# Kernel tuning notes

Hardware: AMD Instinct MI355X
Metric: run time of the kernel (lower is better)

## Reference

```python
import jax, jax.numpy as jnp
import numpy as np

DEST = 64          # args['output_size']
NET = 256          # network_size = input_size - 3*dest_size
INPUT = NET + 3 * DEST  # 448
B, N = 4, 2048


def setup_inputs() -> dict:
    key = jax.random.key(0)
    ks = jax.random.split(key, 9)
    node_feature = jax.random.normal(ks[0], (B, N, INPUT), jnp.float32)
    adj_forward = jax.random.uniform(ks[1], (B, N, N), jnp.float32)
    adj_backward = jax.random.uniform(ks[2], (B, N, N), jnp.float32)
    s = 1.0 / np.sqrt(2 * DEST)
    Wf = jax.random.normal(ks[3], (2 * DEST, DEST), jnp.float32) * s
    bf = jnp.zeros((DEST,), jnp.float32)
    Wb = jax.random.normal(ks[4], (2 * DEST, DEST), jnp.float32) * s
    bb = jnp.zeros((DEST,), jnp.float32)
    W_emb = jax.random.normal(ks[5], (NET, 2 * DEST), jnp.float32) / np.sqrt(NET)
    b_emb = jnp.zeros((2 * DEST,), jnp.float32)
    return {"node_feature": node_feature, "adj_forward": adj_forward,
            "adj_backward": adj_backward, "Wf": Wf, "bf": bf,
            "Wb": Wb, "bb": bb, "W_emb": W_emb, "b_emb": b_emb}


def _gcn(x, adj, W, b):
    # GCN layer: aggregate neighbors then project. x: [B,N,2d], adj: [B,N,N]
    h = jnp.einsum('bmn,bnf->bmf', adj, x)  # message passing
    return h @ W + b                         # [B,N,d]


def reference(node_feature, adj_forward, adj_backward, Wf, bf, Wb, bb, W_emb, b_emb):
    dyn = node_feature[:, :, :DEST]                 # [B,N,d]
    struct = node_feature[:, :, DEST:3 * DEST]      # [B,N,2d]
    stat = node_feature[:, :, 3 * DEST:]            # [B,N,NET]
    fwd_code = dyn * _gcn(struct, adj_forward, Wf, bf)
    bwd_code = dyn * _gcn(struct, adj_backward, Wb, bb)
    emb = jnp.concatenate((fwd_code, bwd_code), axis=2)  # [B,N,2d]
    gate = jax.nn.sigmoid(stat @ W_emb + b_emb)           # [B,N,2d]
    return emb * gate
```

## Files before the change

### kernel.cpp

```cpp
#include <hip/hip_runtime.h>
#include <hip/hip_bf16.h>
#include <math.h>

#define BB   4
#define NN   2048
#define INPT 448

typedef float f32x4 __attribute__((ext_vector_type(4)));
typedef short s16x8 __attribute__((ext_vector_type(8)));
typedef unsigned int u32;

#define MFMA(a,b,c) __builtin_amdgcn_mfma_f32_16x16x32_bf16((a),(b),(c),0,0,0)

__device__ __align__(16) unsigned short g_WcatF[4*8*64*8];
__device__ __align__(16) unsigned short g_WembF[8*8*64*8];
__device__ __align__(16) unsigned short g_UtF[BB*2*64*4*64*8];
__device__ __align__(16) float          g_G2[BB*NN*128];

__device__ __forceinline__ u32 bf16pk(float a, float b) {
    u32 ua = __builtin_bit_cast(u32, a);
    u32 ub = __builtin_bit_cast(u32, b);
    ua += 0x7fffu + ((ua >> 16) & 1u);
    ub += 0x7fffu + ((ub >> 16) & 1u);
    return (ua >> 16) | (ub & 0xffff0000u);
}
__device__ __forceinline__ unsigned short bf16b(float a) {
    u32 ua = __builtin_bit_cast(u32, a);
    ua += 0x7fffu + ((ua >> 16) & 1u);
    return (unsigned short)(ua >> 16);
}

__global__ void k_weights(const float* __restrict__ Wf, const float* __restrict__ Wb,
                          const float* __restrict__ We) {
    int t = blockIdx.x * 256 + threadIdx.x;
    if (t < 2048) {
        int l = t & 63, jf = (t >> 6) & 7, kg = t >> 9;
        int j  = jf * 16 + (l & 15);
        int f0 = kg * 32 + (l >> 4) * 8;
        union { u32 u[4]; s16x8 s; } r;
        #pragma unroll
        for (int e = 0; e < 8; e += 2) {
            float v0 = (j < 64) ? Wf[(f0 + e    ) * 64 + j] : Wb[(f0 + e    ) * 64 + (j - 64)];
            float v1 = (j < 64) ? Wf[(f0 + e + 1) * 64 + j] : Wb[(f0 + e + 1) * 64 + (j - 64)];
            r.u[e >> 1] = bf16pk(v0, v1);
        }
        *(s16x8*)&g_WcatF[t * 8] = r.s;
    } else if (t < 2048 + 4096) {
        int idx = t - 2048;
        int l = idx & 63, cf = (idx >> 6) & 7, kg = idx >> 9;
        int c  = cf * 16 + (l & 15);
        int k0 = kg * 32 + (l >> 4) * 8;
        union { u32 u[4]; s16x8 s; } r;
        #pragma unroll
        for (int e = 0; e < 8; e += 2)
            r.u[e >> 1] = bf16pk(We[(k0 + e) * 128 + c], We[(k0 + e + 1) * 128 + c]);
        *(s16x8*)&g_WembF[idx * 8] = r.s;
    }
}

__global__ __launch_bounds__(256) void k_prep(const float* __restrict__ nfeat,
                                              const float* __restrict__ bemb) {
    __shared__ __align__(16) char sm[24576];
    int tid = threadIdx.x;
    int w = tid >> 6, l = tid & 63, lr = l & 15, lc = l >> 4;
    int bid = blockIdx.x;

    if (bid < 256) {
        int b = bid >> 6, nb = bid & 63;
        unsigned short* ss = (unsigned short*)sm;
        unsigned short* ob = (unsigned short*)(sm + 8192);
        const float* base = nfeat + (size_t)(b * NN + nb * 32) * INPT;
        #pragma unroll
        for (int i = 0; i < 4; ++i) {
            int node = w * 8 + i * 2 + (l >> 5);
            int c4 = (l & 31) * 4;
            float4 v = *(const float4*)(base + (size_t)node * INPT + 64 + c4);
            int off = node * 256 + c4 * 2; off ^= (node & 7) << 4;
            uint2 pk; pk.x = bf16pk(v.x, v.y); pk.y = bf16pk(v.z, v.w);
            *(uint2*)((char*)ss + off) = pk;
        }
        __syncthreads();
        f32x4 acc[2][2] = {};
        #pragma unroll
        for (int kg = 0; kg < 4; ++kg) {
            s16x8 a0 = *(const s16x8*)&g_WcatF[((kg * 8 + w * 2 + 0) * 64 + l) * 8];
            s16x8 a1 = *(const s16x8*)&g_WcatF[((kg * 8 + w * 2 + 1) * 64 + l) * 8];
            #pragma unroll
            for (int na = 0; na < 2; ++na) {
                int off = (na * 16 + lr) * 256 + kg * 64 + lc * 16; off ^= (lr & 7) << 4;
                s16x8 bf = *(const s16x8*)((char*)ss + off);
                acc[0][na] = MFMA(a0, bf, acc[0][na]);
                acc[1][na] = MFMA(a1, bf, acc[1][na]);
            }
        }
        #pragma unroll
        for (int ja = 0; ja < 2; ++ja)
            #pragma unroll
            for (int na = 0; na < 2; ++na)
                #pragma unroll
                for (int r = 0; r < 4; ++r) {
                    int j = w * 32 + ja * 16 + lc * 4 + r;
                    int n = na * 16 + lr;
                    ob[j * 32 + n] = bf16b(acc[ja][na][r]);
                }
        __syncthreads();
        #pragma unroll
        for (int q = 0; q < 2; ++q) {
            int idx = q * 256 + tid;
            int dirx = idx >> 8, nf = (idx >> 6) & 3, ll = idx & 63;
            int j = dirx * 64 + nf * 16 + (ll & 15);
            int n0 = (ll >> 4) * 8;
            s16x8 v = *(const s16x8*)&ob[j * 32 + n0];
            *(s16x8*)&g_UtF[((((size_t)(b * 2 + dirx) * 64 + nb) * 4 + nf) * 64 + ll) * 8] = v;
        }
    } else {
        int bid2 = bid - 256;
        int b = bid2 >> 6, mb = bid2 & 63;
        unsigned short* ss = (unsigned short*)sm;
        float* dyls = (float*)(sm + 16384);
        const float* base = nfeat + (size_t)(b * NN + mb * 32) * INPT;
        #pragma unroll
        for (int i = 0; i < 8; ++i) {
            int row = w * 8 + i;
            float4 v = *(const float4*)(base + (size_t)row * INPT + 192 + l * 4);
            int off = row * 512 + l * 8; off ^= (row & 7) << 4;
            uint2 pk; pk.x = bf16pk(v.x, v.y); pk.y = bf16pk(v.z, v.w);
            *(uint2*)((char*)ss + off) = pk;
        }
        #pragma unroll
        for (int i = 0; i < 2; ++i) {
            int row = w * 8 + i * 4 + lc;
            float4 v = *(const float4*)(base + (size_t)row * INPT + lr * 4);
            *(float4*)&dyls[row * 64 + lr * 4] = v;
        }
        __syncthreads();
        f32x4 acc[2][2] = {};
        #pragma unroll
        for (int kg = 0; kg < 8; ++kg) {
            s16x8 a0, a1;
            {
                int off = lr * 512 + kg * 64 + lc * 16; off ^= (lr & 7) << 4;
                a0 = *(const s16x8*)((char*)ss + off);
                a1 = *(const s16x8*)((char*)ss + off + 8192);
            }
            #pragma unroll
            for (int cfi = 0; cfi < 2; ++cfi) {
                s16x8 bf = *(const s16x8*)&g_WembF[((kg * 8 + w * 2 + cfi) * 64 + l) * 8];
                acc[cfi][0] = MFMA(a0, bf, acc[cfi][0]);
                acc[cfi][1] = MFMA(a1, bf, acc[cfi][1]);
            }
        }
        #pragma unroll
        for (int cfi = 0; cfi < 2; ++cfi) {
            int c = (w * 2 + cfi) * 16 + lr;
            float be = bemb[c];
            #pragma unroll
            for (int mf = 0; mf < 2; ++mf)
                #pragma unroll
                for (int r = 0; r < 4; ++r) {
                    int m = mf * 16 + lc * 4 + r;
                    float v = acc[cfi][mf][r] + be;
                    float g = 1.0f / (1.0f + expf(-v));
                    g_G2[(size_t)(b * NN + mb * 32 + m) * 128 + c] = g * dyls[m * 64 + (c & 63)];
                }
        }
    }
}

#define GLOAD(dst, p) \
    asm volatile("global_load_dwordx4 %0, %1, off" : "=v"(dst) : "v"(p) : "memory")

__global__ __launch_bounds__(256) void k_main(const float* __restrict__ adjf,
                                              const float* __restrict__ adjb,
                                              const float* __restrict__ biasf,
                                              const float* __restrict__ biasb,
                                              float* __restrict__ out) {
    __shared__ __align__(16) char sm[20480];
    int tid = threadIdx.x;
    int w = tid >> 6, l = tid & 63, lr = l & 15, lc = l >> 4;

    int hw  = blockIdx.x;
    int bid = (hw & 7) * 128 + (hw >> 3);
    int tile = bid & 127, dir = (bid >> 7) & 1, b = bid >> 8;

    const float* adj  = dir ? adjb : adjf;
    const float* bias = dir ? biasb : biasf;
    int m0 = tile * 16;
    const unsigned short* utF = g_UtF + (size_t)(b * 2 + dir) * 131072;

    int arow = tid >> 4;
    int u8   = tid & 15;
    const float* asrc = adj + (size_t)(b * NN + m0 + arow) * NN + u8 * 4;
    int awoff = arow * 128 + ((((u8 >> 1) ^ (arow & 7)) << 4)) + (u8 & 1) * 8;
    const unsigned short* bs0 = utF + (size_t)w * 512 + l * 8;
    const unsigned short* bs1 = bs0 + 2048;
    int boff0 = (w * 64 + l) * 16;
    int boff1 = ((4 + w) * 64 + l) * 16;

    f32x4 acc = {};

    {
        f32x4 a0, bv0, bv1;
        GLOAD(a0, asrc);
        GLOAD(bv0, bs0);
        GLOAD(bv1, bs1);
        asm volatile("s_waitcnt vmcnt(0)" : "+v"(a0), "+v"(bv0), "+v"(bv1) : : "memory");
        uint2 pk; pk.x = bf16pk(a0[0], a0[1]); pk.y = bf16pk(a0[2], a0[3]);
        *(uint2*)(sm + awoff) = pk;
        *(f32x4*)(sm + 4096 + boff0) = bv0;
        *(f32x4*)(sm + 4096 + boff1) = bv1;
    }
    __syncthreads();

    for (int t = 0; t < 32; ++t) {
        f32x4 an, bn0, bn1;
        bool pre = (t < 31);
        if (pre) {
            GLOAD(an,  asrc + (t + 1) * 64);
            GLOAD(bn0, bs0 + (t + 1) * 4096);
            GLOAD(bn1, bs1 + (t + 1) * 4096);
        }
        char* Ab = sm + (t & 1) * 2048;
        char* Bb = sm + 4096 + (t & 1) * 8192;
        #pragma unroll
        for (int kk = 0; kk < 2; ++kk) {
            s16x8 af = *(const s16x8*)(Ab + lr * 128 + (((kk * 4 + lc) ^ (lr & 7)) << 4));
            s16x8 bf = *(const s16x8*)(Bb + ((kk * 4 + w) * 64 + l) * 16);
            acc = MFMA(af, bf, acc);
        }
        if (pre) {
            asm volatile("s_waitcnt vmcnt(0)" : "+v"(an), "+v"(bn0), "+v"(bn1) : : "memory");
            char* Ab2 = sm + ((t + 1) & 1) * 2048;
            char* Bb2 = sm + 4096 + ((t + 1) & 1) * 8192;
            uint2 pk; pk.x = bf16pk(an[0], an[1]); pk.y = bf16pk(an[2], an[3]);
            *(uint2*)(Ab2 + awoff) = pk;
            *(f32x4*)(Bb2 + boff0) = bn0;
            *(f32x4*)(Bb2 + boff1) = bn1;
        }
        __syncthreads();
    }

    int col = w * 16 + lr;
    float bv = bias[col];
    #pragma unroll
    for (int r = 0; r < 4; ++r) {
        int mrow = m0 + lc * 4 + r;
        size_t o = (size_t)(b * NN + mrow) * 128 + dir * 64 + col;
        out[o] = (acc[r] + bv) * g_G2[o];
    }
}

extern "C" void kernel_launch(void* const* d_in, const int* in_sizes, int n_in,
                              void* d_out, int out_size, void* d_ws, size_t ws_size,
                              hipStream_t stream) {
    (void)in_sizes; (void)n_in; (void)d_ws; (void)ws_size; (void)out_size;
    const float* nfeat = (const float*)d_in[0];
    const float* adjf  = (const float*)d_in[1];
    const float* adjb  = (const float*)d_in[2];
    const float* Wf    = (const float*)d_in[3];
    const float* bf    = (const float*)d_in[4];
    const float* Wb    = (const float*)d_in[5];
    const float* bb    = (const float*)d_in[6];
    const float* We    = (const float*)d_in[7];
    const float* bemb  = (const float*)d_in[8];
    float* out = (float*)d_out;

    hipLaunchKernelGGL(k_weights, dim3(24),   dim3(256), 0, stream, Wf, Wb, We);
    hipLaunchKernelGGL(k_prep,    dim3(512),  dim3(256), 0, stream, nfeat, bemb);
    hipLaunchKernelGGL(k_main,    dim3(1024), dim3(256), 0, stream, adjf, adjb, bf, bb, out);
}
```

Before: 183.7 us.

## Deepen k_main load pipeline to a 4-stage ring with direct-to-LDS B loads

Replaces the double-buffered loop, which waited on vmcnt(0) every step, with a 4-slot shared-memory ring that keeps three k-stages of loads in flight. It waits with a counted vmcnt and uses a single barrier per step. The B operand (pre-packed bf16) now goes straight from global memory to LDS via global_load_lds, which skips the register round trip. The adjacency A tile is still loaded into registers, converted to bf16 and stored to LDS. LDS use doubles to 40 KB and the launch bounds request 4 blocks per SM, so occupancy may be limited by LDS.

```diff
diff --git a/kernel.cpp b/kernel.cpp
--- a/kernel.cpp
+++ b/kernel.cpp
@@ -167,15 +167,45 @@
     }
 }
 
-#define GLOAD(dst, p) \
+#define GLOADR(dst, p) \
     asm volatile("global_load_dwordx4 %0, %1, off" : "=v"(dst) : "v"(p) : "memory")
 
-__global__ __launch_bounds__(256) void k_main(const float* __restrict__ adjf,
-                                              const float* __restrict__ adjb,
-                                              const float* __restrict__ biasf,
-                                              const float* __restrict__ biasb,
-                                              float* __restrict__ out) {
-    __shared__ __align__(16) char sm[20480];
+#define GL_LDS(g, lptr) \
+    __builtin_amdgcn_global_load_lds((const __attribute__((address_space(1))) void*)(g), \
+                                     (__attribute__((address_space(3))) void*)(lptr), 16, 0, 0)
+
+#define STAGE(s) do { \
+    GLOADR(av[(s) & 3], ap + (size_t)(s) * 64); \
+    GL_LDS(bp + (size_t)(s) * 4096,        smB + ((s) & 3) * 8192 + w * 1024); \
+    GL_LDS(bp + (size_t)(s) * 4096 + 2048, smB + ((s) & 3) * 8192 + (4 + w) * 1024); \
+} while (0)
+
+#define KSTEP(t, vmN, DO_ISSUE) do { \
+    asm volatile("s_waitcnt vmcnt(" #vmN ")" : "+v"(av[(t) & 3]) : : "memory"); \
+    { uint2 pk_; \
+      pk_.x = bf16pk(av[(t) & 3][0], av[(t) & 3][1]); \
+      pk_.y = bf16pk(av[(t) & 3][2], av[(t) & 3][3]); \
+      *(uint2*)(smA + ((t) & 3) * 2048 + awoff) = pk_; } \
+    asm volatile("s_waitcnt lgkmcnt(0)" ::: "memory"); \
+    __builtin_amdgcn_s_barrier(); \
+    __builtin_amdgcn_sched_barrier(0); \
+    if (DO_ISSUE) STAGE((t) + 3); \
+    { char* Ab_ = smA + ((t) & 3) * 2048; \
+      char* Bb_ = smB + ((t) & 3) * 8192; \
+      _Pragma("unroll") \
+      for (int kk = 0; kk < 2; ++kk) { \
+          s16x8 af_ = *(const s16x8*)(Ab_ + lr * 128 + (((kk * 4 + lc) ^ (lr & 7)) << 4)); \
+          s16x8 bf_ = *(const s16x8*)(Bb_ + (kk * 4 + w) * 1024 + l * 16); \
+          acc = MFMA(af_, bf_, acc); \
+      } } \
+} while (0)
+
+__global__ __launch_bounds__(256, 4) void k_main(const float* __restrict__ adjf,
+                                                 const float* __restrict__ adjb,
+                                                 const float* __restrict__ biasf,
+                                                 const float* __restrict__ biasb,
+                                                 float* __restrict__ out) {
+    __shared__ __align__(16) char sm[40960];
     int tid = threadIdx.x;
     int w = tid >> 6, l = tid & 63, lr = l & 15, lc = l >> 4;
 
@@ -190,55 +220,27 @@
 
     int arow = tid >> 4;
     int u8   = tid & 15;
-    const float* asrc = adj + (size_t)(b * NN + m0 + arow) * NN + u8 * 4;
-    int awoff = arow * 128 + ((((u8 >> 1) ^ (arow & 7)) << 4)) + (u8 & 1) * 8;
-    const unsigned short* bs0 = utF + (size_t)w * 512 + l * 8;
-    const unsigned short* bs1 = bs0 + 2048;
-    int boff0 = (w * 64 + l) * 16;
-    int boff1 = ((4 + w) * 64 + l) * 16;
-
+    const float* ap = adj + (size_t)(b * NN + m0 + arow) * NN + u8 * 4;
+    int awoff = arow * 128 + (((u8 >> 1) ^ (arow & 7)) << 4) + (u8 & 1) * 8;
+    const unsigned short* bp = utF + (size_t)w * 512 + (size_t)l * 8;
+    char* smA = sm;
+    char* smB = sm + 8192;
+
+    f32x4 av[4];
     f32x4 acc = {};
 
-    {
-        f32x4 a0, bv0, bv1;
-        GLOAD(a0, asrc);
-        GLOAD(bv0, bs0);
-        GLOAD(bv1, bs1);
-        asm volatile("s_waitcnt vmcnt(0)" : "+v"(a0), "+v"(bv0), "+v"(bv1) : : "memory");
-        uint2 pk; pk.x = bf16pk(a0[0], a0[1]); pk.y = bf16pk(a0[2], a0[3]);
-        *(uint2*)(sm + awoff) = pk;
-        *(f32x4*)(sm + 4096 + boff0) = bv0;
-        *(f32x4*)(sm + 4096 + boff1) = bv1;
-    }
-    __syncthreads();
-
-    for (int t = 0; t < 32; ++t) {
-        f32x4 an, bn0, bn1;
-        bool pre = (t < 31);
-        if (pre) {
-            GLOAD(an,  asrc + (t + 1) * 64);
-            GLOAD(bn0, bs0 + (t + 1) * 4096);
-            GLOAD(bn1, bs1 + (t + 1) * 4096);
-        }
-        char* Ab = sm + (t & 1) * 2048;
-        char* Bb = sm + 4096 + (t & 1) * 8192;
-        #pragma unroll
-        for (int kk = 0; kk < 2; ++kk) {
-            s16x8 af = *(const s16x8*)(Ab + lr * 128 + (((kk * 4 + lc) ^ (lr & 7)) << 4));
-            s16x8 bf = *(const s16x8*)(Bb + ((kk * 4 + w) * 64 + l) * 16);
-            acc = MFMA(af, bf, acc);
-        }
-        if (pre) {
-            asm volatile("s_waitcnt vmcnt(0)" : "+v"(an), "+v"(bn0), "+v"(bn1) : : "memory");
-            char* Ab2 = sm + ((t + 1) & 1) * 2048;
-            char* Bb2 = sm + 4096 + ((t + 1) & 1) * 8192;
-            uint2 pk; pk.x = bf16pk(an[0], an[1]); pk.y = bf16pk(an[2], an[3]);
-            *(uint2*)(Ab2 + awoff) = pk;
-            *(f32x4*)(Bb2 + boff0) = bn0;
-            *(f32x4*)(Bb2 + boff1) = bn1;
-        }
-        __syncthreads();
-    }
+    STAGE(0); STAGE(1); STAGE(2);
+
+    for (int to = 0; to < 7; ++to) {
+        int tb = to * 4;
+        #pragma unroll
+        for (int j = 0; j < 4; ++j)
+            KSTEP(tb + j, 6, true);
+    }
+    KSTEP(28, 6, true);
+    KSTEP(29, 6, false);
+    KSTEP(30, 3, false);
+    KSTEP(31, 0, false);
 
     int col = w * 16 + lr;
     float bv = bias[col];
```

Result: slower. 192.3 us (+4.7%).
